# Kernel optimization log

Measured on AMD Instinct MI355X. Metric: run time of the kernel, lower is better.

The kernel has to match this reference:

```python
import jax, jax.numpy as jnp
import numpy as np

D_MODEL = 768
N_HEADS = 12
HEAD_DIM = D_MODEL // N_HEADS
NEG = -10000.0


def setup_inputs() -> dict:
    key = jax.random.key(0)
    ks = jax.random.split(key, 8)
    B, S, D = 2, 2048, D_MODEL
    inp = {
        "q": jax.random.normal(ks[0], (B, S, D), dtype=jnp.float32),
        "k": jax.random.normal(ks[1], (B, S, D), dtype=jnp.float32),
        "v": jax.random.normal(ks[2], (B, S, D), dtype=jnp.float32),
        "attn_mask": jax.random.randint(ks[3], (B, S), 0, 2, dtype=jnp.int32),
        # weights stored [in, out]; apply as x @ W (equivalent to torch Linear)
        "Wq": jax.random.normal(ks[4], (D, D), dtype=jnp.float32) / np.sqrt(D),
        "Wk": jax.random.normal(ks[5], (D, D), dtype=jnp.float32) / np.sqrt(D),
        "Wv": jax.random.normal(ks[6], (D, D), dtype=jnp.float32) / np.sqrt(D),
        "Wo": jax.random.normal(ks[7], (D, D), dtype=jnp.float32) / np.sqrt(D),
        "mask_future": 1,
    }
    return inp


def reference(q, k, v, attn_mask, Wq, Wk, Wv, Wo, mask_future):
    B, S, D = q.shape
    H, hd = N_HEADS, HEAD_DIM
    # project and split heads -> [B, H, S, hd]
    qh = (q @ Wq).reshape(B, S, H, hd).transpose(0, 2, 1, 3)
    kh = (k @ Wk).reshape(B, S, H, hd).transpose(0, 2, 1, 3)
    vh = (v @ Wv).reshape(B, S, H, hd).transpose(0, 2, 1, 3)

    scale = 1.0 / np.sqrt(hd).astype(np.float32)
    # full [B, H, L, S] score matrix (naive SDPA, as in the original)
    scores = jnp.einsum("bhld,bhsd->bhls", qh, kh) * scale
    if mask_future:
        causal = jnp.triu(jnp.full((S, S), NEG, dtype=scores.dtype), k=1)
        scores = scores + causal
    # padding mask: [B, S] -> broadcast over heads and query positions
    pad = attn_mask[:, None, None, :] == 0
    scores = jnp.where(pad, NEG, scores)
    attn = jax.nn.softmax(scores, axis=-1)  # dropout p=0.0 -> identity
    out = jnp.einsum("bhls,bhsd->bhld", attn, vh)  # [B, H, L, hd]
    out = out.transpose(0, 2, 1, 3).reshape(B, S, D)
    return out @ Wo
```

## Files before the change

### kernel.cpp

```cpp
#include <hip/hip_runtime.h>


#define NEGV (-10000.0f)

typedef __attribute__((ext_vector_type(8))) short v8s;
typedef __attribute__((ext_vector_type(4))) float v4f;
typedef __attribute__((ext_vector_type(8))) unsigned short v8u;

#define GLDS16(g, l)                                            \
  __builtin_amdgcn_global_load_lds(                             \
      (const __attribute__((address_space(1))) void*)(g),       \
      (__attribute__((address_space(3))) void*)(l), 16, 0, 0)

__device__ __forceinline__ unsigned short f2bf(float f) {
  unsigned int u = __float_as_uint(f);
  u += 0x7FFFu + ((u >> 16) & 1u);
  return (unsigned short)(u >> 16);
}

__device__ __forceinline__ unsigned int cvt_pk_bf16(float lo, float hi) {
  unsigned int r;
  asm("v_cvt_pk_bf16_f32 %0, %1, %2" : "=v"(r) : "v"(lo), "v"(hi));
  return r;
}

__global__ __launch_bounds__(256) void transpose_w(
    const float* __restrict__ w0, const float* __restrict__ w1,
    const float* __restrict__ w2, const float* __restrict__ w3,
    unsigned short* __restrict__ t0, unsigned short* __restrict__ t1,
    unsigned short* __restrict__ t2, unsigned short* __restrict__ t3) {
  const float* w; unsigned short* t;
  switch (blockIdx.z) {
    case 0: w = w0; t = t0; break;
    case 1: w = w1; t = t1; break;
    case 2: w = w2; t = t2; break;
    default: w = w3; t = t3; break;
  }
  __shared__ unsigned short tile[32][33];
  const int tx = threadIdx.x & 31, ty = threadIdx.x >> 5;
  const int x0 = blockIdx.x * 32, y0 = blockIdx.y * 32;
#pragma unroll
  for (int j = 0; j < 4; j++)
    tile[ty + j * 8][tx] = f2bf(w[(size_t)(y0 + ty + j * 8) * 768 + x0 + tx]);
  __syncthreads();
#pragma unroll
  for (int j = 0; j < 4; j++)
    t[(size_t)(x0 + ty + j * 8) * 768 + y0 + tx] = tile[tx][ty + j * 8];
}

__global__ __launch_bounds__(256) void transpose_vh(
    const unsigned short* __restrict__ vh, unsigned short* __restrict__ vht) {
  __shared__ unsigned short tile[32][33];
  const size_t hoff = (size_t)blockIdx.z * 2048 * 64;
  const unsigned short* src = vh + hoff;
  unsigned short* dst = vht + hoff;
  const int s0 = blockIdx.x * 32, d0 = blockIdx.y * 32;
  const int tx = threadIdx.x & 31, ty = threadIdx.x >> 5;
#pragma unroll
  for (int j = 0; j < 4; j++)
    tile[ty + j * 8][tx] = src[(size_t)(s0 + ty + j * 8) * 64 + d0 + tx];
  __syncthreads();
#pragma unroll
  for (int j = 0; j < 4; j++)
    dst[(size_t)(d0 + ty + j * 8) * 2048 + s0 + tx] = tile[tx][ty + j * 8];
}

template <bool ABF16HEAD, bool CF32ROW>
__device__ __forceinline__ void gemm_core(const void* __restrict__ A,
                                          const unsigned short* __restrict__ Wt,
                                          void* __restrict__ C) {
  const int tid = threadIdx.x;
  const int wave = tid >> 6, lane = tid & 63;
  const int quad = lane >> 4, l16 = lane & 15;
  const int wm = wave >> 1, wn = wave & 1;
  const int bm = blockIdx.x * 128, bn = blockIdx.y * 128;

  __shared__ __align__(16) unsigned short As[2][128 * 32];
  __shared__ __align__(16) unsigned short Bs[2][128 * 32];

  const int r0s = tid >> 2, c0s = (tid & 3) << 3;

  v4f acc[4][4];
#pragma unroll
  for (int i = 0; i < 4; i++)
#pragma unroll
    for (int j = 0; j < 4; j++) acc[i][j] = (v4f){0.f, 0.f, 0.f, 0.f};

  float4 nA00, nA01, nA10, nA11;

  auto issueB = [&](int kt, int nb) {
    const int c = kt * 32 + c0s;
    GLDS16(&Wt[(size_t)(bn + r0s) * 768 + c],
           &Bs[nb][(size_t)(wave * 64) * 8]);
    GLDS16(&Wt[(size_t)(bn + r0s + 64) * 768 + c],
           &Bs[nb][(size_t)(256 + wave * 64) * 8]);
  };
  auto issueA_glds = [&](int kt, int nb) {
    const int c = kt * 32 + c0s;
    const int rg0 = bm + r0s, rg1 = bm + r0s + 64;
    size_t a0 = ((size_t)((rg0 >> 11) * 12 + (c >> 6)) * 2048 +
                 (rg0 & 2047)) * 64 + (c & 63);
    size_t a1 = ((size_t)((rg1 >> 11) * 12 + (c >> 6)) * 2048 +
                 (rg1 & 2047)) * 64 + (c & 63);
    GLDS16((const unsigned short*)A + a0, &As[nb][(size_t)(wave * 64) * 8]);
    GLDS16((const unsigned short*)A + a1,
           &As[nb][(size_t)(256 + wave * 64) * 8]);
  };
  auto issueA_f32 = [&](int kt) {
    const float* Af = (const float*)A;
    const int c = kt * 32 + c0s;
    size_t a0 = (size_t)(bm + r0s) * 768 + c;
    size_t a1 = (size_t)(bm + r0s + 64) * 768 + c;
    nA00 = *(const float4*)(Af + a0);
    nA01 = *(const float4*)(Af + a0 + 4);
    nA10 = *(const float4*)(Af + a1);
    nA11 = *(const float4*)(Af + a1 + 4);
  };
  auto writeA_f32 = [&](int nb) {
    v8u t0, t1;
    t0[0] = f2bf(nA00.x); t0[1] = f2bf(nA00.y);
    t0[2] = f2bf(nA00.z); t0[3] = f2bf(nA00.w);
    t0[4] = f2bf(nA01.x); t0[5] = f2bf(nA01.y);
    t0[6] = f2bf(nA01.z); t0[7] = f2bf(nA01.w);
    t1[0] = f2bf(nA10.x); t1[1] = f2bf(nA10.y);
    t1[2] = f2bf(nA10.z); t1[3] = f2bf(nA10.w);
    t1[4] = f2bf(nA11.x); t1[5] = f2bf(nA11.y);
    t1[6] = f2bf(nA11.z); t1[7] = f2bf(nA11.w);
    *(uint4*)&As[nb][r0s * 32 + c0s] = *(uint4*)&t0;
    *(uint4*)&As[nb][(r0s + 64) * 32 + c0s] = *(uint4*)&t1;
  };

  if (ABF16HEAD) {
    issueA_glds(0, 0);
  } else {
    issueA_f32(0);
  }
  issueB(0, 0);
  if (!ABF16HEAD) writeA_f32(0);
  __syncthreads();

  for (int kt = 0; kt < 24; kt++) {
    const int cur = kt & 1, nxt = cur ^ 1;

    if (kt < 23) {
      if (ABF16HEAD) issueA_glds(kt + 1, nxt);
      else issueA_f32(kt + 1);
      issueB(kt + 1, nxt);
    }

    v8s aF[4], bF[4];
#pragma unroll
    for (int mt = 0; mt < 4; mt++)
      aF[mt] =
          *(const v8s*)&As[cur][(wm * 64 + mt * 16 + l16) * 32 + quad * 8];
#pragma unroll
    for (int nt = 0; nt < 4; nt++)
      bF[nt] =
          *(const v8s*)&Bs[cur][(wn * 64 + nt * 16 + l16) * 32 + quad * 8];
#pragma unroll
    for (int mt = 0; mt < 4; mt++)
#pragma unroll
      for (int nt = 0; nt < 4; nt++)
        acc[mt][nt] = __builtin_amdgcn_mfma_f32_16x16x32_bf16(
            aF[mt], bF[nt], acc[mt][nt], 0, 0, 0);

    if (kt < 23 && !ABF16HEAD) writeA_f32(nxt);
    __syncthreads();
  }

#pragma unroll
  for (int mt = 0; mt < 4; mt++) {
#pragma unroll
    for (int i = 0; i < 4; i++) {
      int row = bm + wm * 64 + mt * 16 + quad * 4 + i;
#pragma unroll
      for (int nt = 0; nt < 4; nt++) {
        int col = bn + wn * 64 + nt * 16 + l16;
        if (CF32ROW) {
          ((float*)C)[(size_t)row * 768 + col] = acc[mt][nt][i];
        } else {
          size_t off = ((size_t)((row >> 11) * 12 + (col >> 6)) * 2048 +
                        (row & 2047)) * 64 + (col & 63);
          ((unsigned short*)C)[off] = f2bf(acc[mt][nt][i]);
        }
      }
    }
  }
}

__global__ __launch_bounds__(256) void gemm_qkv(
    const float* __restrict__ xq, const float* __restrict__ xk,
    const float* __restrict__ xv, const unsigned short* __restrict__ wqt,
    const unsigned short* __restrict__ wkt, const unsigned short* __restrict__ wvt,
    unsigned short* __restrict__ qh, unsigned short* __restrict__ kh,
    unsigned short* __restrict__ vh) {
  const float* A; const unsigned short* Wt; unsigned short* C;
  switch (blockIdx.z) {
    case 0: A = xq; Wt = wqt; C = qh; break;
    case 1: A = xk; Wt = wkt; C = kh; break;
    default: A = xv; Wt = wvt; C = vh; break;
  }
  gemm_core<false, false>((const void*)A, Wt, (void*)C);
}

__global__ __launch_bounds__(256) void gemm_o(
    const unsigned short* __restrict__ oat, const unsigned short* __restrict__ wot,
    float* __restrict__ out) {
  gemm_core<true, true>((const void*)oat, wot, (void*)out);
}

__global__ __launch_bounds__(256) void attn_kernel(
    const unsigned short* __restrict__ qh, const unsigned short* __restrict__ kh,
    const unsigned short* __restrict__ vht, const int* __restrict__ attn_mask,
    const int* __restrict__ mask_future, unsigned short* __restrict__ o) {
  const int S = 2048, HD = 64, NH = 12;

  const int nlin = blockIdx.x + 32 * blockIdx.y;
  const int m_ = nlin & 255, t_ = nlin >> 8;
  const int i_ = (t_ == 1) ? (511 - m_) : (t_ * 256 + m_);
  const int qt = 31 - i_ / 24;
  const int bh = i_ - (i_ / 24) * 24;
  const int b = bh / NH, h = bh % NH;

  const int tid = threadIdx.x;
  const int wave = tid >> 6, lane = tid & 63;
  const int quad = lane >> 4, l16 = lane & 15;

  __shared__ __align__(16) unsigned short Ks[2][64 * 72];
  __shared__ __align__(16) unsigned short Vt[2][64 * 72];
  __shared__ __align__(16) unsigned short Ps[4][16 * 72];
  __shared__ int s_flag;

  const size_t head_off = (size_t)(b * NH + h) * S * HD;
  const unsigned short* Kb = kh + head_off;
  const unsigned short* Vb = vht + head_off;

  const int mf = mask_future[0];
  if (tid == 0) s_flag = 0;

  const int qrow_l = qt * 64 + wave * 16 + l16;
  v8s aQ[2];
  {
    const unsigned short* qp = qh + head_off + (size_t)qrow_l * HD + quad * 8;
    aQ[0] = *(const v8s*)(qp);
    aQ[1] = *(const v8s*)(qp + 32);
  }
  const int qbase_D = qt * 64 + wave * 16 + quad * 4;

  float m_i = -1e30f;
  v4f accO[4], accL;
  accL = (v4f){0.f, 0.f, 0.f, 0.f};
#pragma unroll
  for (int dt = 0; dt < 4; dt++) accO[dt] = (v4f){0.f, 0.f, 0.f, 0.f};

  v8s ones;
#pragma unroll
  for (int j = 0; j < 8; j++) ones[j] = (short)0x3F80;

  const int kt_causal = mf ? qt : (S / 64 - 1);
  const int r0 = tid >> 3, c0s = (tid & 7) << 3;

  auto nexttile = [&](int t) -> int {
    if (t < kt_causal) return t + 1;
    if (t == kt_causal) return (mf && kt_causal < S / 64 - 1) ? t + 1 : -1;
    return (t < S / 64 - 1) ? t + 1 : -1;
  };

  uint4 pk0, pk1, pv0, pv1;
  int pmv = 0;
  unsigned long long msk0 = 0, msk1 = 0;
  int rtile = -1, stile = -1;

  auto prefetch = [&](int kt) {
    const uint4* srck = (const uint4*)(Kb + (size_t)kt * 64 * HD);
    pk0 = srck[tid];
    pk1 = srck[256 + tid];
    const unsigned short* vp = Vb + (size_t)r0 * S + kt * 64 + c0s;
    pv0 = *(const uint4*)vp;
    pv1 = *(const uint4*)(vp + (size_t)32 * S);
    pmv = attn_mask[b * S + kt * 64 + lane];
    rtile = kt;
  };

  auto stage = [&](int kb) {
    *(uint4*)&Ks[kb][r0 * 72 + c0s] = pk0;
    *(uint4*)&Ks[kb][(r0 + 32) * 72 + c0s] = pk1;
    *(uint4*)&Vt[kb][r0 * 72 + c0s] = pv0;
    *(uint4*)&Vt[kb][(r0 + 32) * 72 + c0s] = pv1;
    unsigned long long mk = __ballot(pmv != 0);
    if (kb) msk1 = mk; else msk0 = mk;
  };

  for (int phase = 0; phase < 2; phase++) {
    int kt_lo, kt_hi;
    if (phase == 0) { kt_lo = 0; kt_hi = kt_causal; }
    else {
      if (m_i < -5000.f) s_flag = 1;
      __syncthreads();
      if (!s_flag) break;
      kt_lo = kt_causal + 1; kt_hi = S / 64 - 1;
      if (kt_lo > kt_hi) break;
    }

    if (stile != kt_lo) {
      if (rtile != kt_lo) prefetch(kt_lo);
      stage(kt_lo & 1);
      stile = kt_lo;
      int nx = nexttile(kt_lo);
      if (nx >= 0) prefetch(nx);
    }

    for (int kt = kt_lo; kt <= kt_hi; kt++) {
      __syncthreads();

      int nkt = nexttile(kt);
      if (nkt >= 0 && stile != nkt) {
        stage(nkt & 1);
        stile = nkt;
        int n2 = nexttile(nkt);
        if (n2 >= 0) prefetch(n2);
      }

      const int kb = kt & 1;
      const unsigned short* KsB = Ks[kb];
      const unsigned short* VtB = Vt[kb];
      const unsigned long long mk = kb ? msk1 : msk0;

      v4f sc[4];
      __builtin_amdgcn_s_setprio(1);
#pragma unroll
      for (int nt = 0; nt < 4; nt++) {
        const unsigned short* kp = &KsB[(nt * 16 + l16) * 72 + quad * 8];
        v8s k0 = *(const v8s*)kp;
        v8s k1 = *(const v8s*)(kp + 32);
        v4f z = (v4f){0.f, 0.f, 0.f, 0.f};
        z = __builtin_amdgcn_mfma_f32_16x16x32_bf16(k0, aQ[0], z, 0, 0, 0);
        z = __builtin_amdgcn_mfma_f32_16x16x32_bf16(k1, aQ[1], z, 0, 0, 0);
        sc[nt] = z;
      }
      __builtin_amdgcn_s_setprio(0);

#pragma unroll
      for (int nt = 0; nt < 4; nt++) {
#pragma unroll
        for (int i = 0; i < 4; i++) {
          int kid = nt * 16 + quad * 4 + i;
          int key = kt * 64 + kid;
          float v = sc[nt][i] * 0.125f;
          v += (mf && (key > qrow_l)) ? NEGV : 0.f;
          v = ((mk >> kid) & 1ull) ? v : NEGV;
          sc[nt][i] = v;
        }
      }

      float mx;
      {
        float a = fmaxf(fmaxf(sc[0][0], sc[0][1]), fmaxf(sc[0][2], sc[0][3]));
        float b2 = fmaxf(fmaxf(sc[1][0], sc[1][1]), fmaxf(sc[1][2], sc[1][3]));
        float c = fmaxf(fmaxf(sc[2][0], sc[2][1]), fmaxf(sc[2][2], sc[2][3]));
        float d = fmaxf(fmaxf(sc[3][0], sc[3][1]), fmaxf(sc[3][2], sc[3][3]));
        mx = fmaxf(fmaxf(a, b2), fmaxf(c, d));
      }
      mx = fmaxf(mx, __shfl_xor(mx, 16));
      mx = fmaxf(mx, __shfl_xor(mx, 32));

      if (!__all(mx - m_i <= 8.0f)) {
        float mnew = fmaxf(m_i, mx);
        float alpha = __expf(m_i - mnew);
        m_i = mnew;
        float a0 = __shfl(alpha, quad * 4 + 0);
        float a1 = __shfl(alpha, quad * 4 + 1);
        float a2 = __shfl(alpha, quad * 4 + 2);
        float a3 = __shfl(alpha, quad * 4 + 3);
#pragma unroll
        for (int dt = 0; dt < 4; dt++) {
          accO[dt][0] *= a0; accO[dt][1] *= a1;
          accO[dt][2] *= a2; accO[dt][3] *= a3;
        }
        accL[0] *= a0; accL[1] *= a1; accL[2] *= a2; accL[3] *= a3;
      }

#pragma unroll
      for (int nt = 0; nt < 4; nt++) {
#pragma unroll
        for (int i = 0; i < 4; i++)
          sc[nt][i] = __expf(sc[nt][i] - m_i);
        uint2 w;
        w.x = cvt_pk_bf16(sc[nt][0], sc[nt][1]);
        w.y = cvt_pk_bf16(sc[nt][2], sc[nt][3]);
        *(uint2*)&Ps[wave][l16 * 72 + nt * 16 + quad * 4] = w;
      }

      __builtin_amdgcn_s_setprio(1);
#pragma unroll
      for (int ks = 0; ks < 2; ks++) {
        v8s aP = *(const v8s*)&Ps[wave][l16 * 72 + ks * 32 + quad * 8];
        accL = __builtin_amdgcn_mfma_f32_16x16x32_bf16(aP, ones, accL, 0, 0, 0);
#pragma unroll
        for (int dt = 0; dt < 4; dt++) {
          v8s bV = *(const v8s*)&VtB[(dt * 16 + l16) * 72 + ks * 32 + quad * 8];
          accO[dt] =
              __builtin_amdgcn_mfma_f32_16x16x32_bf16(aP, bV, accO[dt], 0, 0, 0);
        }
      }
      __builtin_amdgcn_s_setprio(0);
    }
    if (phase == 0) __syncthreads();
  }

#pragma unroll
  for (int i = 0; i < 4; i++) {
    float inv = 1.f / accL[i];
    int qr = qbase_D + i;
    size_t base = head_off + (size_t)qr * HD;
#pragma unroll
    for (int dt = 0; dt < 4; dt++)
      o[base + dt * 16 + l16] = f2bf(accO[dt][i] * inv);
  }
}

extern "C" void kernel_launch(void* const* d_in, const int* in_sizes, int n_in,
                              void* d_out, int out_size, void* d_ws, size_t ws_size,
                              hipStream_t stream) {
  const float* q  = (const float*)d_in[0];
  const float* k  = (const float*)d_in[1];
  const float* v  = (const float*)d_in[2];
  const int* amask = (const int*)d_in[3];
  const float* Wq = (const float*)d_in[4];
  const float* Wk = (const float*)d_in[5];
  const float* Wv = (const float*)d_in[6];
  const float* Wo = (const float*)d_in[7];
  const int* mf  = (const int*)d_in[8];
  float* out = (float*)d_out;

  unsigned short* ws = (unsigned short*)d_ws;
  unsigned short* qh = ws;
  unsigned short* kh = qh + 3145728;
  unsigned short* vh = kh + 3145728;
  unsigned short* wqt = vh + 3145728;
  unsigned short* wkt = wqt + 589824;
  unsigned short* wvt = wkt + 589824;
  unsigned short* wot = wvt + 589824;
  unsigned short* vht = (unsigned short*)d_out;

  transpose_w<<<dim3(24, 24, 4), 256, 0, stream>>>(Wq, Wk, Wv, Wo,
                                                   wqt, wkt, wvt, wot);
  gemm_qkv<<<dim3(32, 6, 3), 256, 0, stream>>>(q, k, v, wqt, wkt, wvt,
                                               qh, kh, vh);
  transpose_vh<<<dim3(64, 2, 24), 256, 0, stream>>>(vh, vht);
  attn_kernel<<<dim3(32, 24), 256, 0, stream>>>(qh, kh, vht, amask, mf, qh);
  gemm_o<<<dim3(32, 6), 256, 0, stream>>>(qh, wot, out);
}
```

Before: 210.7 us.

## Replace global_load_lds with register-staged double-buffered loads and lighter barriers

```diff
diff --git a/kernel.cpp b/kernel.cpp
--- a/kernel.cpp
+++ b/kernel.cpp
@@ -7,10 +7,12 @@
 typedef __attribute__((ext_vector_type(4))) float v4f;
 typedef __attribute__((ext_vector_type(8))) unsigned short v8u;
 
-#define GLDS16(g, l)                                            \
-  __builtin_amdgcn_global_load_lds(                             \
-      (const __attribute__((address_space(1))) void*)(g),       \
-      (__attribute__((address_space(3))) void*)(l), 16, 0, 0)
+#define BAR()                                                   \
+  do {                                                          \
+    asm volatile("s_waitcnt lgkmcnt(0)" ::: "memory");          \
+    __builtin_amdgcn_s_barrier();                               \
+    __builtin_amdgcn_sched_barrier(0);                          \
+  } while (0)
 
 __device__ __forceinline__ unsigned short f2bf(float f) {
   unsigned int u = __float_as_uint(f);
@@ -86,68 +88,59 @@
 #pragma unroll
     for (int j = 0; j < 4; j++) acc[i][j] = (v4f){0.f, 0.f, 0.f, 0.f};
 
-  float4 nA00, nA01, nA10, nA11;
-
-  auto issueB = [&](int kt, int nb) {
+  struct Stg {
+    float4 a00, a01, a10, a11;
+    uint4 ha0, ha1;
+    uint4 b0, b1;
+  };
+  Stg s0, s1;
+
+  auto loadS = [&](Stg& s, int kt) {
     const int c = kt * 32 + c0s;
-    GLDS16(&Wt[(size_t)(bn + r0s) * 768 + c],
-           &Bs[nb][(size_t)(wave * 64) * 8]);
-    GLDS16(&Wt[(size_t)(bn + r0s + 64) * 768 + c],
-           &Bs[nb][(size_t)(256 + wave * 64) * 8]);
-  };
-  auto issueA_glds = [&](int kt, int nb) {
-    const int c = kt * 32 + c0s;
-    const int rg0 = bm + r0s, rg1 = bm + r0s + 64;
-    size_t a0 = ((size_t)((rg0 >> 11) * 12 + (c >> 6)) * 2048 +
-                 (rg0 & 2047)) * 64 + (c & 63);
-    size_t a1 = ((size_t)((rg1 >> 11) * 12 + (c >> 6)) * 2048 +
-                 (rg1 & 2047)) * 64 + (c & 63);
-    GLDS16((const unsigned short*)A + a0, &As[nb][(size_t)(wave * 64) * 8]);
-    GLDS16((const unsigned short*)A + a1,
-           &As[nb][(size_t)(256 + wave * 64) * 8]);
-  };
-  auto issueA_f32 = [&](int kt) {
-    const float* Af = (const float*)A;
-    const int c = kt * 32 + c0s;
-    size_t a0 = (size_t)(bm + r0s) * 768 + c;
-    size_t a1 = (size_t)(bm + r0s + 64) * 768 + c;
-    nA00 = *(const float4*)(Af + a0);
-    nA01 = *(const float4*)(Af + a0 + 4);
-    nA10 = *(const float4*)(Af + a1);
-    nA11 = *(const float4*)(Af + a1 + 4);
-  };
-  auto writeA_f32 = [&](int nb) {
-    v8u t0, t1;
-    t0[0] = f2bf(nA00.x); t0[1] = f2bf(nA00.y);
-    t0[2] = f2bf(nA00.z); t0[3] = f2bf(nA00.w);
-    t0[4] = f2bf(nA01.x); t0[5] = f2bf(nA01.y);
-    t0[6] = f2bf(nA01.z); t0[7] = f2bf(nA01.w);
-    t1[0] = f2bf(nA10.x); t1[1] = f2bf(nA10.y);
-    t1[2] = f2bf(nA10.z); t1[3] = f2bf(nA10.w);
-    t1[4] = f2bf(nA11.x); t1[5] = f2bf(nA11.y);
-    t1[6] = f2bf(nA11.z); t1[7] = f2bf(nA11.w);
-    *(uint4*)&As[nb][r0s * 32 + c0s] = *(uint4*)&t0;
-    *(uint4*)&As[nb][(r0s + 64) * 32 + c0s] = *(uint4*)&t1;
-  };
-
-  if (ABF16HEAD) {
-    issueA_glds(0, 0);
-  } else {
-    issueA_f32(0);
-  }
-  issueB(0, 0);
-  if (!ABF16HEAD) writeA_f32(0);
-  __syncthreads();
-
-  for (int kt = 0; kt < 24; kt++) {
-    const int cur = kt & 1, nxt = cur ^ 1;
-
-    if (kt < 23) {
-      if (ABF16HEAD) issueA_glds(kt + 1, nxt);
-      else issueA_f32(kt + 1);
-      issueB(kt + 1, nxt);
-    }
-
+    if (ABF16HEAD) {
+      const unsigned short* Ah = (const unsigned short*)A;
+      const int rg0 = bm + r0s, rg1 = bm + r0s + 64;
+      size_t a0 = ((size_t)((rg0 >> 11) * 12 + (c >> 6)) * 2048 +
+                   (rg0 & 2047)) * 64 + (c & 63);
+      size_t a1 = ((size_t)((rg1 >> 11) * 12 + (c >> 6)) * 2048 +
+                   (rg1 & 2047)) * 64 + (c & 63);
+      s.ha0 = *(const uint4*)(Ah + a0);
+      s.ha1 = *(const uint4*)(Ah + a1);
+    } else {
+      const float* Af = (const float*)A;
+      size_t a0 = (size_t)(bm + r0s) * 768 + c;
+      size_t a1 = (size_t)(bm + r0s + 64) * 768 + c;
+      s.a00 = *(const float4*)(Af + a0);
+      s.a01 = *(const float4*)(Af + a0 + 4);
+      s.a10 = *(const float4*)(Af + a1);
+      s.a11 = *(const float4*)(Af + a1 + 4);
+    }
+    s.b0 = *(const uint4*)&Wt[(size_t)(bn + r0s) * 768 + c];
+    s.b1 = *(const uint4*)&Wt[(size_t)(bn + r0s + 64) * 768 + c];
+  };
+
+  auto writeS = [&](Stg& s, int nb) {
+    if (ABF16HEAD) {
+      *(uint4*)&As[nb][r0s * 32 + c0s] = s.ha0;
+      *(uint4*)&As[nb][(r0s + 64) * 32 + c0s] = s.ha1;
+    } else {
+      v8u t0, t1;
+      t0[0] = f2bf(s.a00.x); t0[1] = f2bf(s.a00.y);
+      t0[2] = f2bf(s.a00.z); t0[3] = f2bf(s.a00.w);
+      t0[4] = f2bf(s.a01.x); t0[5] = f2bf(s.a01.y);
+      t0[6] = f2bf(s.a01.z); t0[7] = f2bf(s.a01.w);
+      t1[0] = f2bf(s.a10.x); t1[1] = f2bf(s.a10.y);
+      t1[2] = f2bf(s.a10.z); t1[3] = f2bf(s.a10.w);
+      t1[4] = f2bf(s.a11.x); t1[5] = f2bf(s.a11.y);
+      t1[6] = f2bf(s.a11.z); t1[7] = f2bf(s.a11.w);
+      *(uint4*)&As[nb][r0s * 32 + c0s] = *(uint4*)&t0;
+      *(uint4*)&As[nb][(r0s + 64) * 32 + c0s] = *(uint4*)&t1;
+    }
+    *(uint4*)&Bs[nb][r0s * 32 + c0s] = s.b0;
+    *(uint4*)&Bs[nb][(r0s + 64) * 32 + c0s] = s.b1;
+  };
+
+  auto compute = [&](int cur) {
     v8s aF[4], bF[4];
 #pragma unroll
     for (int mt = 0; mt < 4; mt++)
@@ -163,9 +156,22 @@
       for (int nt = 0; nt < 4; nt++)
         acc[mt][nt] = __builtin_amdgcn_mfma_f32_16x16x32_bf16(
             aF[mt], bF[nt], acc[mt][nt], 0, 0, 0);
-
-    if (kt < 23 && !ABF16HEAD) writeA_f32(nxt);
-    __syncthreads();
+  };
+
+  loadS(s0, 0);
+  loadS(s1, 1);
+  writeS(s0, 0);
+  BAR();
+
+  for (int kt = 0; kt < 24; kt += 2) {
+    if (kt + 2 < 24) loadS(s0, kt + 2);
+    writeS(s1, 1);
+    compute(0);
+    BAR();
+    if (kt + 3 < 24) loadS(s1, kt + 3);
+    if (kt + 2 < 24) writeS(s0, 0);
+    compute(1);
+    BAR();
   }
 
 #pragma unroll
@@ -311,7 +317,7 @@
     }
 
     for (int kt = kt_lo; kt <= kt_hi; kt++) {
-      __syncthreads();
+      BAR();
 
       int nkt = nexttile(kt);
       if (nkt >= 0 && stile != nkt) {
```

Result: slower. 247.1 us (+17.3%).
